# Kernel tuning notes

Measured on AMD Instinct MI355X. Metric: run time of the kernel, lower is better.

## Reference

```python
import jax, jax.numpy as jnp
import numpy as np

N_R, N_V, D, E_RR, L, G = 50000, 2000, 128, 800000, 3, 32


def setup_inputs() -> dict:
    key = jax.random.key(0)
    ks = jax.random.split(key, 10)
    x_real = jax.random.normal(ks[0], (N_R, D), dtype=jnp.float32)
    x_virtual = jax.random.normal(ks[1], (N_V, D), dtype=jnp.float32)
    # params: [num_layers, 3 relations (r_to_r, r_to_v, v_to_r), D, D]
    W_root = jax.random.normal(ks[2], (L, 3, D, D), dtype=jnp.float32) * 0.05
    W_nbr = jax.random.normal(ks[3], (L, 3, D, D), dtype=jnp.float32) * 0.05
    bias = jax.random.normal(ks[4], (L, 3, D), dtype=jnp.float32) * 0.05
    edge_rr = jax.random.randint(ks[5], (2, E_RR), 0, N_R)
    # one virtual-node edge per real node (hierarchical virtual nodes)
    src_rv = jnp.arange(N_R)
    dst_rv = jax.random.randint(ks[6], (N_R,), 0, N_V)
    edge_rv = jnp.stack([src_rv, dst_rv])          # real -> virtual
    edge_vr = jnp.stack([dst_rv, src_rv])          # virtual -> real
    batch_real = jnp.sort(jax.random.randint(ks[7], (N_R,), 0, G))
    return {
        "x_real": x_real, "x_virtual": x_virtual,
        "W_root": W_root, "W_nbr": W_nbr, "bias": bias,
        "edge_rr": edge_rr, "edge_rv": edge_rv, "edge_vr": edge_vr,
        "batch_real": batch_real,
    }


def _graph_conv(x_src, x_dst, src, dst, Wr, Wn, b, n_dst):
    # PyG GraphConv-style: root transform + sum-aggregated neighbor messages
    msg = jax.ops.segment_sum(x_src[src] @ Wn, dst, num_segments=n_dst)
    return x_dst @ Wr + msg + b


def _forward(x_real, x_virtual, W_root, W_nbr, bias, edge_rr, edge_rv, edge_vr, batch_real):
    x_r, x_v = x_real, x_virtual
    n_r, n_v = x_r.shape[0], x_v.shape[0]
    for l in range(W_root.shape[0]):
        # HeteroConv with aggr='sum': sum relation outputs per destination type
        c_rr = _graph_conv(x_r, x_r, edge_rr[0], edge_rr[1], W_root[l, 0], W_nbr[l, 0], bias[l, 0], n_r)
        c_vr = _graph_conv(x_v, x_r, edge_vr[0], edge_vr[1], W_root[l, 2], W_nbr[l, 2], bias[l, 2], n_r)
        c_rv = _graph_conv(x_r, x_v, edge_rv[0], edge_rv[1], W_root[l, 1], W_nbr[l, 1], bias[l, 1], n_v)
        # activation + dropout (eval mode -> identity)
        x_r = jax.nn.relu(c_rr + c_vr)
        x_v = jax.nn.relu(c_rv)
    # mean readout over real nodes per graph
    counts = jax.ops.segment_sum(jnp.ones((n_r,), x_r.dtype), batch_real, num_segments=G)
    graph_emb = jax.ops.segment_sum(x_r, batch_real, num_segments=G) / jnp.maximum(counts, 1.0)[:, None]
    return x_r, graph_emb


def reference(x_real, x_virtual, W_root, W_nbr, bias, edge_rr, edge_rv, edge_vr, batch_real):
    node_embedding, graph_embedding = _forward(
        x_real, x_virtual, W_root, W_nbr, bias, edge_rr, edge_rv, edge_vr, batch_real)
    return node_embedding, graph_embedding
```

## Files before the change

### kernel.cpp

```cpp
#include <hip/hip_runtime.h>
#include <hip/hip_bf16.h>

#define N_R   50000
#define N_V   2000
#define DIM   128
#define E_RR  800000
#define EPAD  (E_RR + 4 * N_R)
#define NLAY  3
#define NGR   32
#define RCHUNK 16

#define BUKD  128
#define NBUK  391
#define CHKE  2048
#define NCHK  391

typedef __attribute__((ext_vector_type(8))) short bf16x8;
typedef __attribute__((ext_vector_type(4))) float f32x4;
typedef __attribute__((ext_vector_type(2))) float f32x2;
typedef __attribute__((ext_vector_type(8))) unsigned char u8x8;

__device__ __forceinline__ ushort f2bf(float f) {
    unsigned u = __builtin_bit_cast(unsigned, f);
    unsigned r = (u + 0x7fffu + ((u >> 16) & 1u)) >> 16;
    return (ushort)r;
}
__device__ __forceinline__ float bf2f(ushort h) {
    unsigned u = ((unsigned)h) << 16;
    return __builtin_bit_cast(float, u);
}
__device__ __forceinline__ int lbound(const int* __restrict__ a, int n, int key) {
    int lo = 0, hi = n;
    while (lo < hi) { int mid = (lo + hi) >> 1; if (a[mid] < key) lo = mid + 1; else hi = mid; }
    return lo;
}

__device__ __forceinline__ void acc_u8row(
    unsigned w0, unsigned w1, float s,
    f32x2& a01, f32x2& a23, f32x2& a45, f32x2& a67)
{
    f32x2 sc = {s, s};
    a01 += sc * (f32x2){(float)(w0 & 0xffu), (float)((w0 >> 8) & 0xffu)};
    a23 += sc * (f32x2){(float)((w0 >> 16) & 0xffu), (float)(w0 >> 24)};
    a45 += sc * (f32x2){(float)(w1 & 0xffu), (float)((w1 >> 8) & 0xffu)};
    a67 += sc * (f32x2){(float)((w1 >> 16) & 0xffu), (float)(w1 >> 24)};
}

__global__ __launch_bounds__(256) void hist_kernel(
    const int* __restrict__ dst, int n, int* __restrict__ cnt)
{
    int i = blockIdx.x * 256 + threadIdx.x;
    if (i < n) atomicAdd(&cnt[dst[i]], 1);
}

__global__ __launch_bounds__(256) void scan_single_kernel(
    const int* __restrict__ cnt, int n, int nedges,
    int* __restrict__ rowptr, int* __restrict__ cursor)
{
    __shared__ int lds[256];
    __shared__ int carry;
    int t = threadIdx.x;
    if (t == 0) carry = 0;
    __syncthreads();
    for (int base = 0; base < n; base += 256) {
        int i = base + t;
        int v = (i < n) ? cnt[i] : 0;
        lds[t] = v;
        __syncthreads();
        #pragma unroll
        for (int off = 1; off < 256; off <<= 1) {
            int u = (t >= off) ? lds[t - off] : 0;
            __syncthreads();
            lds[t] += u;
            __syncthreads();
        }
        int excl = carry + lds[t] - v;
        if (i < n) {
            rowptr[i] = excl;
            if (cursor) cursor[i] = excl;
        }
        __syncthreads();
        if (t == 255) carry += lds[255];
        __syncthreads();
    }
    if (t == 0) rowptr[n] = (nedges >= 0) ? nedges : carry;
}

__global__ __launch_bounds__(256) void fill_kernel(
    const int* __restrict__ src, const int* __restrict__ dst, int n,
    int* __restrict__ cursor, int* __restrict__ col)
{
    int i = blockIdx.x * 256 + threadIdx.x;
    if (i < n) {
        int p = atomicAdd(&cursor[dst[i]], 1);
        col[p] = src[i];
    }
}

__global__ __launch_bounds__(256) void bkt_count_kernel(
    const int* __restrict__ dst, unsigned short* __restrict__ cnt2d)
{
    __shared__ int h[NBUK];
    int t = threadIdx.x, c = blockIdx.x;
    for (int i = t; i < NBUK; i += 256) h[i] = 0;
    __syncthreads();
    int e0 = c * CHKE, e1 = min(e0 + CHKE, E_RR);
    for (int e = e0 + t; e < e1; e += 256) atomicAdd(&h[dst[e] >> 7], 1);
    __syncthreads();
    for (int i = t; i < NBUK; i += 256)
        cnt2d[(size_t)c * NBUK + i] = (unsigned short)h[i];
}

__global__ __launch_bounds__(64) void bkt_prefix_kernel(
    const unsigned short* __restrict__ cnt2d,
    unsigned short* __restrict__ rel2d, int* __restrict__ tot)
{
    int b = blockIdx.x, lane = threadIdx.x;
    int base = 0;
    for (int c0 = 0; c0 < NCHK; c0 += 64) {
        int c = c0 + lane;
        int v = (c < NCHK) ? (int)cnt2d[(size_t)c * NBUK + b] : 0;
        int s = v;
        #pragma unroll
        for (int off = 1; off < 64; off <<= 1) {
            int u = __shfl_up(s, off);
            if (lane >= off) s += u;
        }
        if (c < NCHK) rel2d[(size_t)c * NBUK + b] = (unsigned short)(base + s - v);
        base += __shfl(s, 63);
    }
    if (lane == 0) tot[b] = base;
}

__global__ __launch_bounds__(256) void bkt_scatter_kernel(
    const int* __restrict__ src, const int* __restrict__ dst,
    const unsigned short* __restrict__ rel2d, const int* __restrict__ bstart,
    unsigned* __restrict__ ebuf)
{
    __shared__ int cur[NBUK];
    int t = threadIdx.x, c = blockIdx.x;
    for (int i = t; i < NBUK; i += 256)
        cur[i] = bstart[i] + (int)rel2d[(size_t)c * NBUK + i];
    __syncthreads();
    int e0 = c * CHKE, e1 = min(e0 + CHKE, E_RR);
    for (int e = e0 + t; e < e1; e += 256) {
        int d = dst[e];
        int p = atomicAdd(&cur[d >> 7], 1);
        ebuf[p] = ((unsigned)d << 16) | (unsigned)src[e];
    }
}

__global__ __launch_bounds__(256) void bkt_fineA_kernel(
    const unsigned* __restrict__ ebuf, const int* __restrict__ bstart,
    unsigned short* __restrict__ rowcnt, int* __restrict__ ptot)
{
    __shared__ int cnt[BUKD];
    __shared__ int red[BUKD];
    int b = blockIdx.x, t = threadIdx.x;
    int s0 = bstart[b], s1 = bstart[b + 1];
    if (t < BUKD) cnt[t] = 0;
    __syncthreads();
    for (int e = s0 + t; e < s1; e += 256)
        atomicAdd(&cnt[(ebuf[e] >> 16) & (BUKD - 1)], 1);
    __syncthreads();
    if (t < BUKD) {
        rowcnt[(size_t)b * BUKD + t] = (unsigned short)cnt[t];
        red[t] = (cnt[t] + 3) & ~3;
    }
    __syncthreads();
    #pragma unroll
    for (int off = 64; off > 0; off >>= 1) {
        if (t < off) red[t] += red[t + off];
        __syncthreads();
    }
    if (t == 0) ptot[b] = red[0];
}

__global__ __launch_bounds__(256) void bkt_fineB_kernel(
    const unsigned* __restrict__ ebuf, const int* __restrict__ bstart,
    const int* __restrict__ pbstart, const unsigned short* __restrict__ rowcnt,
    int* __restrict__ rowptr, unsigned short* __restrict__ col16)
{
    __shared__ int sc[BUKD];
    __shared__ int cur[BUKD];
    __shared__ int fend[BUKD];
    __shared__ int pend[BUKD];
    int b = blockIdx.x, t = threadIdx.x;
    int s0 = bstart[b], s1 = bstart[b + 1];
    int p0 = pbstart[b];
    int c = (t < BUKD) ? (int)rowcnt[(size_t)b * BUKD + t] : 0;
    int pc = (c + 3) & ~3;
    if (t < BUKD) sc[t] = pc;
    __syncthreads();
    #pragma unroll
    for (int off = 1; off < BUKD; off <<= 1) {
        int v = (t < BUKD && t >= off) ? sc[t - off] : 0;
        __syncthreads();
        if (t < BUKD) sc[t] += v;
        __syncthreads();
    }
    if (t < BUKD) {
        int ex = sc[t] - pc;
        int d = b * BUKD + t;
        if (d < N_R) rowptr[d] = p0 + ex;
        cur[t] = ex;
        fend[t] = ex + c;
        pend[t] = ex + pc;
    }
    if (b == NBUK - 1 && t == 0) rowptr[N_R] = pbstart[NBUK];
    __syncthreads();
    for (int e = s0 + t; e < s1; e += 256) {
        unsigned pk = ebuf[e];
        int p = atomicAdd(&cur[(pk >> 16) & (BUKD - 1)], 1);
        col16[p0 + p] = (unsigned short)(pk & 0xffffu);
    }
    __syncthreads();
    if (t < BUKD) {
        for (int p = fend[t]; p < pend[t]; ++p)
            col16[p0 + p] = 0xFFFFu;
    }
}

__global__ __launch_bounds__(256) void quant_input_kernel(
    const float* __restrict__ in, unsigned char* __restrict__ q,
    unsigned short* __restrict__ sbf)
{
    int w = (blockIdx.x * 256 + threadIdx.x) >> 6;
    int lane = threadIdx.x & 63;
    if (w >= N_R) return;
    float2 v = *(const float2*)(in + (size_t)w * DIM + lane * 2);
    float mx = fmaxf(fabsf(v.x), fabsf(v.y));
    #pragma unroll
    for (int off = 1; off < 64; off <<= 1)
        mx = fmaxf(mx, __shfl_xor(mx, off));
    ushort sb = f2bf(mx / 127.f);
    float s = bf2f(sb);
    float inv = (s > 0.f) ? 1.f / s : 0.f;
    int q0 = min(255, max(0, __float2int_rn(v.x * inv) + 128));
    int q1 = min(255, max(0, __float2int_rn(v.y * inv) + 128));
    *(ushort*)(q + (size_t)w * DIM + lane * 2) = (ushort)(q0 | (q1 << 8));
    if (lane == 0) sbf[w] = sb;
}

__global__ __launch_bounds__(256) void build_wt_kernel(
    const float* __restrict__ Wroot, const float* __restrict__ Wnbr,
    ushort* __restrict__ WT)
{
    int idx = blockIdx.x * 256 + threadIdx.x;
    if (idx >= NLAY * DIM * 2 * DIM) return;
    int k = idx & 255;
    int n = (idx >> 8) & 127;
    int l = idx >> 15;
    float v;
    if (k < DIM) {
        const float* base = Wroot + (size_t)l * 3 * DIM * DIM;
        v = base[(size_t)k * DIM + n] + base[(size_t)(2 * DIM + k) * DIM + n];
    } else {
        v = Wnbr[((size_t)l * 3 * DIM + (k - DIM)) * DIM + n];
    }
    WT[idx] = f2bf(v);
}

__global__ __launch_bounds__(256) void combine_b_kernel(
    const float* __restrict__ bias, float* __restrict__ bc)
{
    int idx = blockIdx.x * 256 + threadIdx.x;
    if (idx >= NLAY * DIM) return;
    int l = idx / DIM;
    int rest = idx - l * DIM;
    const float* base = bias + (size_t)l * 3 * DIM;
    bc[idx] = base[rest] + base[2 * DIM + rest];
}

__global__ __launch_bounds__(256) void vlayer_kernel(
    const int* __restrict__ rowptr_rr, const unsigned short* __restrict__ col16,
    unsigned* __restrict__ colp,
    const int* __restrict__ rowptr, const int* __restrict__ col,
    const unsigned char* __restrict__ Xq, const unsigned short* __restrict__ sbf,
    float zp, const float* __restrict__ xv,
    const float* __restrict__ Wn2, const float* __restrict__ Wr1,
    const float* __restrict__ Wn1, const float* __restrict__ b1,
    float* __restrict__ Tv, float* __restrict__ xv_next, int doNext)
{
    __shared__ float part[4 * DIM];
    __shared__ float arv_s[DIM];
    int v = blockIdx.x;
    int t = threadIdx.x;
    int wave = t >> 6, lane = t & 63;

    {
        int ptot = rowptr_rr[N_R];
        for (int i = v * 256 + t; i < ptot; i += N_V * 256) {
            unsigned c = col16[i];
            colp[i] = (c == 0xFFFFu) ? 0u : (c | ((unsigned)sbf[c] << 16));
        }
    }

    if (doNext) {
        int beg = rowptr[v], end = rowptr[v + 1];
        float a0 = 0.f, a1 = 0.f, ssum = 0.f;
        for (int e = beg + wave; e < end; e += 4) {
            int c = col[e];
            float s = bf2f(sbf[c]);
            uchar2 u = *(const uchar2*)(Xq + (size_t)c * DIM + lane * 2);
            a0 += s * (float)u.x;
            a1 += s * (float)u.y;
            ssum += s;
        }
        part[wave * DIM + lane * 2 + 0] = a0 - zp * ssum;
        part[wave * DIM + lane * 2 + 1] = a1 - zp * ssum;
        __syncthreads();
        if (t < DIM)
            arv_s[t] = part[t] + part[DIM + t] + part[2 * DIM + t] + part[3 * DIM + t];
        __syncthreads();
    }

    const float* arow = xv + (size_t)v * DIM;
    if (t < DIM) {
        float tacc = 0.f;
        #pragma unroll 8
        for (int k = 0; k < DIM; ++k)
            tacc += arow[k] * Wn2[(size_t)k * DIM + t];
        Tv[(size_t)v * DIM + t] = tacc;
    } else if (doNext) {
        int c = t - DIM;
        float nacc = 0.f;
        #pragma unroll 4
        for (int k = 0; k < DIM; ++k)
            nacc += arow[k] * Wr1[(size_t)k * DIM + c]
                  + arv_s[k] * Wn1[(size_t)k * DIM + c];
        xv_next[(size_t)v * DIM + c] = fmaxf(nacc + b1[c], 0.f);
    }
}

__global__ __launch_bounds__(256) void fused_layer_kernel(
    const int* __restrict__ rowptr, const unsigned* __restrict__ colp,
    const unsigned char* __restrict__ Xq, const unsigned short* __restrict__ sbf,
    float zp, const ushort* __restrict__ WT,
    const float* __restrict__ Tv,  const int* __restrict__ vmap,
    const float* __restrict__ bias,
    float* __restrict__ outF,
    unsigned char* __restrict__ Xq_out, unsigned short* __restrict__ sbf_out, int M)
{
    __shared__ ushort a2[16 * DIM];
    __shared__ float ost[16 * DIM];
    int t = threadIdx.x;

    int wave = t >> 6, lane = t & 63;
    int rlo = lane & 15, hi = lane >> 4;
    int row0 = blockIdx.x * 16;
    int arowc = min(row0 + rlo, M - 1);
    float sa = bf2f(sbf[arowc]);
    bf16x8 afr[8];
    #pragma unroll
    for (int j = 0; j < 4; ++j) {
        u8x8 uv = *(const u8x8*)(Xq + (size_t)arowc * DIM + 32 * j + 8 * hi);
        bf16x8 f;
        #pragma unroll
        for (int q = 0; q < 8; ++q)
            f[q] = (short)f2bf(sa * ((float)uv[q] - zp));
        afr[j] = f;
    }
    int vr[4];
    #pragma unroll
    for (int i = 0; i < 4; ++i)
        vr[i] = vmap[min(row0 + 4 * hi + i, M - 1)];

    {
        int g = t >> 3;
        int li = t & 7;
        int row = g >> 1;
        int half = g & 1;
        int drow = min(row0 + row, M - 1);
        int beg = rowptr[drow], end = rowptr[drow + 1];
        const unsigned char* XH = Xq + half * 64 + li * 8;
        f32x2 a01 = {0.f, 0.f}, a23 = {0.f, 0.f};
        f32x2 a45 = {0.f, 0.f}, a67 = {0.f, 0.f};
        float ssum = 0.f;
        for (int e = beg; e < end; e += 4) {
            uint4 p = *(const uint4*)(colp + e);
            float s0 = bf2f((ushort)(p.x >> 16)), s1 = bf2f((ushort)(p.y >> 16));
            float s2 = bf2f((ushort)(p.z >> 16)), s3 = bf2f((ushort)(p.w >> 16));
            uint2 d0 = *(const uint2*)(XH + (size_t)(p.x & 0xffffu) * DIM);
            uint2 d1 = *(const uint2*)(XH + (size_t)(p.y & 0xffffu) * DIM);
            uint2 d2 = *(const uint2*)(XH + (size_t)(p.z & 0xffffu) * DIM);
            uint2 d3 = *(const uint2*)(XH + (size_t)(p.w & 0xffffu) * DIM);
            acc_u8row(d0.x, d0.y, s0, a01, a23, a45, a67);
            acc_u8row(d1.x, d1.y, s1, a01, a23, a45, a67);
            acc_u8row(d2.x, d2.y, s2, a01, a23, a45, a67);
            acc_u8row(d3.x, d3.y, s3, a01, a23, a45, a67);
            ssum += (s0 + s1) + (s2 + s3);
        }
        float zs = zp * ssum;
        bf16x8 pk;
        pk[0] = (short)f2bf(a01.x - zs);
        pk[1] = (short)f2bf(a01.y - zs);
        pk[2] = (short)f2bf(a23.x - zs);
        pk[3] = (short)f2bf(a23.y - zs);
        pk[4] = (short)f2bf(a45.x - zs);
        pk[5] = (short)f2bf(a45.y - zs);
        pk[6] = (short)f2bf(a67.x - zs);
        pk[7] = (short)f2bf(a67.y - zs);
        int byte = row * 256 + ((half * 128 + li * 16) ^ ((row & 7) << 4));
        *(bf16x8*)((char*)a2 + byte) = pk;
    }
    __syncthreads();

    #pragma unroll
    for (int jj = 0; jj < 4; ++jj) {
        int byte = rlo * 256 + ((64 * jj + 16 * hi) ^ ((rlo & 7) << 4));
        afr[4 + jj] = *(const bf16x8*)((const char*)a2 + byte);
    }

    f32x4 acc[2];
    #pragma unroll
    for (int n = 0; n < 2; ++n) acc[n] = (f32x4){0.f, 0.f, 0.f, 0.f};

    #pragma unroll
    for (int n = 0; n < 2; ++n) {
        int nt = wave * 2 + n;
        const ushort* wrow = WT + (size_t)(nt * 16 + rlo) * (2 * DIM);
        #pragma unroll
        for (int j = 0; j < 8; ++j) {
            bf16x8 bfr = *(const bf16x8*)(wrow + 32 * j + 8 * hi);
            acc[n] = __builtin_amdgcn_mfma_f32_16x16x32_bf16(afr[j], bfr, acc[n], 0, 0, 0);
        }
    }

    if (outF) {
        #pragma unroll
        for (int n = 0; n < 2; ++n) {
            int ncol = (wave * 2 + n) * 16 + rlo;
            float bv = bias[ncol];
            #pragma unroll
            for (int i = 0; i < 4; ++i) {
                int orow = row0 + 4 * hi + i;
                if (orow >= M) continue;
                float v = acc[n][i] + bv + Tv[(size_t)vr[i] * DIM + ncol];
                outF[(size_t)orow * DIM + ncol] = fmaxf(v, 0.f);
            }
        }
    } else {
        #pragma unroll
        for (int n = 0; n < 2; ++n) {
            int ncol = (wave * 2 + n) * 16 + rlo;
            float bv = bias[ncol];
            #pragma unroll
            for (int i = 0; i < 4; ++i) {
                float v = acc[n][i] + bv + Tv[(size_t)vr[i] * DIM + ncol];
                ost[(4 * hi + i) * DIM + ncol] = fmaxf(v, 0.f);
            }
        }
        __syncthreads();
        int g16 = t >> 4;
        int li16 = t & 15;
        int orow = row0 + g16;
        float4 f0 = *(const float4*)(ost + g16 * DIM + li16 * 8);
        float4 f1 = *(const float4*)(ost + g16 * DIM + li16 * 8 + 4);
        float mx = fmaxf(fmaxf(fmaxf(f0.x, f0.y), fmaxf(f0.z, f0.w)),
                         fmaxf(fmaxf(f1.x, f1.y), fmaxf(f1.z, f1.w)));
        #pragma unroll
        for (int off = 1; off < 16; off <<= 1)
            mx = fmaxf(mx, __shfl_xor(mx, off, 16));
        ushort sb = f2bf(mx / 255.f);
        float s = bf2f(sb);
        float inv = (s > 0.f) ? 1.f / s : 0.f;
        if (orow < M) {
            u8x8 qv;
            qv[0] = (unsigned char)min(255, __float2int_rn(f0.x * inv));
            qv[1] = (unsigned char)min(255, __float2int_rn(f0.y * inv));
            qv[2] = (unsigned char)min(255, __float2int_rn(f0.z * inv));
            qv[3] = (unsigned char)min(255, __float2int_rn(f0.w * inv));
            qv[4] = (unsigned char)min(255, __float2int_rn(f1.x * inv));
            qv[5] = (unsigned char)min(255, __float2int_rn(f1.y * inv));
            qv[6] = (unsigned char)min(255, __float2int_rn(f1.z * inv));
            qv[7] = (unsigned char)min(255, __float2int_rn(f1.w * inv));
            *(u8x8*)(Xq_out + (size_t)orow * DIM + li16 * 8) = qv;
            if (li16 == 0) sbf_out[orow] = sb;
        }
    }
}

__global__ __launch_bounds__(256) void readout_kernel(
    const float* __restrict__ xr, const int* __restrict__ batch,
    float* __restrict__ gsum, int nrows)
{
    __shared__ float lds[256 * 4];
    int g = blockIdx.x / RCHUNK;
    int chunk = blockIdx.x % RCHUNK;
    int lo = lbound(batch, nrows, g);
    int hi = lbound(batch, nrows, g + 1);
    int len = hi - lo;
    if (len == 0) return;
    int per = (len + RCHUNK - 1) / RCHUNK;
    int r0 = lo + chunk * per;
    int r1 = min(r0 + per, hi);

    int t = threadIdx.x;
    int c4 = (t & 31) << 2;
    int rsub = t >> 5;

    float4 acc = make_float4(0.f, 0.f, 0.f, 0.f);
    for (int r = r0 + rsub; r < r1; r += 8) {
        float4 v = *(const float4*)(xr + (size_t)r * DIM + c4);
        acc.x += v.x; acc.y += v.y; acc.z += v.z; acc.w += v.w;
    }
    *(float4*)(lds + t * 4) = acc;
    __syncthreads();
    if (rsub == 0) {
        float4 s = make_float4(0.f, 0.f, 0.f, 0.f);
        #pragma unroll
        for (int j = 0; j < 8; ++j) {
            float4 v = *(const float4*)(lds + (j * 32 + t) * 4);
            s.x += v.x; s.y += v.y; s.z += v.z; s.w += v.w;
        }
        atomicAdd(&gsum[(size_t)g * DIM + c4 + 0], s.x);
        atomicAdd(&gsum[(size_t)g * DIM + c4 + 1], s.y);
        atomicAdd(&gsum[(size_t)g * DIM + c4 + 2], s.z);
        atomicAdd(&gsum[(size_t)g * DIM + c4 + 3], s.w);
    }
}

__global__ __launch_bounds__(256) void finalize_kernel(
    const float* __restrict__ gsum, const int* __restrict__ batch,
    float* __restrict__ out, int nrows)
{
    int idx = blockIdx.x * 256 + threadIdx.x;
    if (idx >= NGR * DIM) return;
    int g = idx >> 7;
    int lo = lbound(batch, nrows, g);
    int hi = lbound(batch, nrows, g + 1);
    float c = fmaxf((float)(hi - lo), 1.f);
    out[idx] = gsum[idx] / c;
}

extern "C" void kernel_launch(void* const* d_in, const int* in_sizes, int n_in,
                              void* d_out, int out_size, void* d_ws, size_t ws_size,
                              hipStream_t stream)
{
    const float* x_real    = (const float*)d_in[0];
    const float* x_virtual = (const float*)d_in[1];
    const float* W_root    = (const float*)d_in[2];
    const float* W_nbr     = (const float*)d_in[3];
    const float* bias      = (const float*)d_in[4];
    const int*   edge_rr   = (const int*)d_in[5];
    const int*   edge_rv   = (const int*)d_in[6];
    const int*   edge_vr   = (const int*)d_in[7];
    const int*   batch     = (const int*)d_in[8];

    float* out = (float*)d_out;

    float*  ws    = (float*)d_ws;
    float*  Tv    = ws;
    float*  xv_a  = Tv   + (size_t)N_V * DIM;
    float*  xv_b  = xv_a + (size_t)N_V * DIM;
    float*  bc    = xv_b + (size_t)N_V * DIM;
    float*  gsum  = bc   + (size_t)NLAY * DIM;
    ushort* WT    = (ushort*)(gsum + NGR * DIM);
    unsigned* colp = (unsigned*)(WT + (size_t)NLAY * DIM * 2 * DIM);
    unsigned* ebuf = colp + EPAD;
    int* iws       = (int*)(ebuf + E_RR);
    int* rowptr_rr = iws;
    int* cnt_v     = rowptr_rr + N_R + 1;
    int* rowptr_rv = cnt_v + N_V;
    int* cursor_rv = rowptr_rv + N_V + 1;
    int* col_rv    = cursor_rv + N_V;
    int* tot       = col_rv + N_R;
    int* bstart    = tot + NBUK;
    int* ptot      = bstart + NBUK + 1;
    int* pbstart   = ptot + NBUK;
    unsigned short* col16 = (unsigned short*)(pbstart + NBUK + 1);
    unsigned short* cnt2d = col16 + EPAD;
    unsigned short* rel2d = cnt2d + (size_t)NCHK * NBUK;
    unsigned short* rowcnt = rel2d + (size_t)NCHK * NBUK;
    unsigned short* sbf0  = rowcnt + (size_t)NBUK * BUKD;
    unsigned short* sbf1  = sbf0 + N_R;
    unsigned short* sbf2  = sbf1 + N_R;
    unsigned char* Q0 = (unsigned char*)(sbf2 + N_R);
    unsigned char* Q1 = Q0 + (size_t)N_R * DIM;
    unsigned char* Q2 = Q1 + (size_t)N_R * DIM;

    const int* rr_src = edge_rr;
    const int* rr_dst = edge_rr + E_RR;
    const int* rv_src = edge_rv;
    const int* rv_dst = edge_rv + N_R;

    bkt_count_kernel<<<NCHK, 256, 0, stream>>>(rr_dst, cnt2d);
    bkt_prefix_kernel<<<NBUK, 64, 0, stream>>>(cnt2d, rel2d, tot);
    scan_single_kernel<<<1, 256, 0, stream>>>(tot, NBUK, E_RR, bstart, nullptr);
    bkt_scatter_kernel<<<NCHK, 256, 0, stream>>>(rr_src, rr_dst, rel2d, bstart, ebuf);
    bkt_fineA_kernel<<<NBUK, 256, 0, stream>>>(ebuf, bstart, rowcnt, ptot);
    scan_single_kernel<<<1, 256, 0, stream>>>(ptot, NBUK, -1, pbstart, nullptr);
    bkt_fineB_kernel<<<NBUK, 256, 0, stream>>>(ebuf, bstart, pbstart, rowcnt,
                                               rowptr_rr, col16);

    hipMemsetAsync(cnt_v, 0, (size_t)N_V * sizeof(int), stream);
    hist_kernel<<<(N_R + 255) / 256, 256, 0, stream>>>(rv_dst, N_R, cnt_v);
    scan_single_kernel<<<1, 256, 0, stream>>>(cnt_v, N_V, N_R, rowptr_rv, cursor_rv);
    fill_kernel<<<(N_R + 255) / 256, 256, 0, stream>>>(rv_src, rv_dst, N_R, cursor_rv, col_rv);

    build_wt_kernel<<<(NLAY * DIM * 2 * DIM + 255) / 256, 256, 0, stream>>>(W_root, W_nbr, WT);
    combine_b_kernel<<<(NLAY * DIM + 255) / 256, 256, 0, stream>>>(bias, bc);
    quant_input_kernel<<<(N_R * 64 + 255) / 256, 256, 0, stream>>>(x_real, Q0, sbf0);

    unsigned char* Qcur = Q0;  unsigned short* Scur = sbf0;
    const float* cur_xv = x_virtual;

    for (int l = 0; l < NLAY; ++l) {
        const float* Wn1 = W_nbr + ((size_t)l * 3 + 1) * DIM * DIM;
        const float* Wn2 = W_nbr + ((size_t)l * 3 + 2) * DIM * DIM;
        const float* Wr1 = W_root + ((size_t)l * 3 + 1) * DIM * DIM;
        const float* b1  = bias + ((size_t)l * 3 + 1) * DIM;

        int doNext = (l < NLAY - 1);
        float zp = (l == 0) ? 128.f : 0.f;
        float* xv_out = (l & 1) ? xv_b : xv_a;

        vlayer_kernel<<<N_V, 256, 0, stream>>>(
            rowptr_rr, col16, colp,
            rowptr_rv, col_rv, Qcur, Scur, zp, cur_xv,
            Wn2, Wr1, Wn1, b1, Tv, xv_out, doNext);

        unsigned char*  Qnext = (l == 0) ? Q1 : Q2;
        unsigned short* Snext = (l == 0) ? sbf1 : sbf2;
        float* outF = (l == NLAY - 1) ? out : nullptr;
        fused_layer_kernel<<<(N_R + 15) / 16, 256, 0, stream>>>(
            rowptr_rr, colp, Qcur, Scur, zp, WT + (size_t)l * DIM * 2 * DIM,
            Tv, edge_vr, bc + (size_t)l * DIM,
            outF, outF ? nullptr : Qnext, outF ? nullptr : Snext, N_R);

        if (doNext) { cur_xv = xv_out; Qcur = Qnext; Scur = Snext; }
    }

    hipMemsetAsync(gsum, 0, (size_t)NGR * DIM * sizeof(float), stream);
    readout_kernel<<<NGR * RCHUNK, 256, 0, stream>>>(out, batch, gsum, N_R);
    finalize_kernel<<<(NGR * DIM + 255) / 256, 256, 0, stream>>>(
        gsum, batch, out + (size_t)N_R * DIM, N_R);
}
```

Measured before the change: 317.4 us.

## Sort destination rows by degree to balance fused layer work

Builds a permutation of real nodes bucketed by in-degree, using a histogram, a scan and an atomic scatter, and makes the fused layer kernel process rows in that order. The aim is that the 16 rows in each block have similar edge counts, so the gather loop wastes less time waiting on its longest row. It adds small preprocessing kernels and indirect row indexing. Row reads and writes become scattered instead of contiguous, which may hurt memory coalescing.

```diff
diff --git a/kernel.cpp b/kernel.cpp
--- a/kernel.cpp
+++ b/kernel.cpp
@@ -218,6 +218,28 @@
     if (t < BUKD) {
         for (int p = fend[t]; p < pend[t]; ++p)
             col16[p0 + p] = 0xFFFFu;
+    }
+}
+
+__global__ __launch_bounds__(256) void deg_hist_kernel(
+    const int* __restrict__ rowptr, int* __restrict__ dh)
+{
+    int i = blockIdx.x * 256 + threadIdx.x;
+    if (i < N_R) {
+        int d = min(255, (rowptr[i + 1] - rowptr[i]) >> 2);
+        atomicAdd(&dh[d], 1);
+    }
+}
+
+__global__ __launch_bounds__(256) void deg_scatter_kernel(
+    const int* __restrict__ rowptr, int* __restrict__ cursor,
+    int* __restrict__ perm)
+{
+    int i = blockIdx.x * 256 + threadIdx.x;
+    if (i < N_R) {
+        int d = min(255, (rowptr[i + 1] - rowptr[i]) >> 2);
+        int p = atomicAdd(&cursor[d], 1);
+        perm[p] = i;
     }
 }
 
@@ -335,6 +357,7 @@
 
 __global__ __launch_bounds__(256) void fused_layer_kernel(
     const int* __restrict__ rowptr, const unsigned* __restrict__ colp,
+    const int* __restrict__ perm,
     const unsigned char* __restrict__ Xq, const unsigned short* __restrict__ sbf,
     float zp, const ushort* __restrict__ WT,
     const float* __restrict__ Tv,  const int* __restrict__ vmap,
@@ -349,7 +372,7 @@
     int wave = t >> 6, lane = t & 63;
     int rlo = lane & 15, hi = lane >> 4;
     int row0 = blockIdx.x * 16;
-    int arowc = min(row0 + rlo, M - 1);
+    int arowc = perm[min(row0 + rlo, M - 1)];
     float sa = bf2f(sbf[arowc]);
     bf16x8 afr[8];
     #pragma unroll
@@ -361,17 +384,20 @@
             f[q] = (short)f2bf(sa * ((float)uv[q] - zp));
         afr[j] = f;
     }
+    int pr[4];
     int vr[4];
     #pragma unroll
-    for (int i = 0; i < 4; ++i)
-        vr[i] = vmap[min(row0 + 4 * hi + i, M - 1)];
+    for (int i = 0; i < 4; ++i) {
+        pr[i] = perm[min(row0 + 4 * hi + i, M - 1)];
+        vr[i] = vmap[pr[i]];
+    }
 
     {
         int g = t >> 3;
         int li = t & 7;
         int row = g >> 1;
         int half = g & 1;
-        int drow = min(row0 + row, M - 1);
+        int drow = perm[min(row0 + row, M - 1)];
         int beg = rowptr[drow], end = rowptr[drow + 1];
         const unsigned char* XH = Xq + half * 64 + li * 8;
         f32x2 a01 = {0.f, 0.f}, a23 = {0.f, 0.f};
@@ -434,10 +460,9 @@
             float bv = bias[ncol];
             #pragma unroll
             for (int i = 0; i < 4; ++i) {
-                int orow = row0 + 4 * hi + i;
-                if (orow >= M) continue;
+                if (row0 + 4 * hi + i >= M) continue;
                 float v = acc[n][i] + bv + Tv[(size_t)vr[i] * DIM + ncol];
-                outF[(size_t)orow * DIM + ncol] = fmaxf(v, 0.f);
+                outF[(size_t)pr[i] * DIM + ncol] = fmaxf(v, 0.f);
             }
         }
     } else {
@@ -454,7 +479,6 @@
         __syncthreads();
         int g16 = t >> 4;
         int li16 = t & 15;
-        int orow = row0 + g16;
         float4 f0 = *(const float4*)(ost + g16 * DIM + li16 * 8);
         float4 f1 = *(const float4*)(ost + g16 * DIM + li16 * 8 + 4);
         float mx = fmaxf(fmaxf(fmaxf(f0.x, f0.y), fmaxf(f0.z, f0.w)),
@@ -465,7 +489,8 @@
         ushort sb = f2bf(mx / 255.f);
         float s = bf2f(sb);
         float inv = (s > 0.f) ? 1.f / s : 0.f;
-        if (orow < M) {
+        if (row0 + g16 < M) {
+            int orow = perm[row0 + g16];
             u8x8 qv;
             qv[0] = (unsigned char)min(255, __float2int_rn(f0.x * inv));
             qv[1] = (unsigned char)min(255, __float2int_rn(f0.y * inv));
@@ -569,7 +594,10 @@
     int* bstart    = tot + NBUK;
     int* ptot      = bstart + NBUK + 1;
     int* pbstart   = ptot + NBUK;
-    unsigned short* col16 = (unsigned short*)(pbstart + NBUK + 1);
+    int* perm      = pbstart + NBUK + 1;
+    int* dh        = perm + N_R;
+    int* dcur      = dh + 257;
+    unsigned short* col16 = (unsigned short*)(dcur + 256);
     unsigned short* cnt2d = col16 + EPAD;
     unsigned short* rel2d = cnt2d + (size_t)NCHK * NBUK;
     unsigned short* rowcnt = rel2d + (size_t)NCHK * NBUK;
@@ -594,6 +622,11 @@
     bkt_fineB_kernel<<<NBUK, 256, 0, stream>>>(ebuf, bstart, pbstart, rowcnt,
                                                rowptr_rr, col16);
 
+    hipMemsetAsync(dh, 0, 257 * sizeof(int), stream);
+    deg_hist_kernel<<<(N_R + 255) / 256, 256, 0, stream>>>(rowptr_rr, dh);
+    scan_single_kernel<<<1, 256, 0, stream>>>(dh, 256, -1, dh, dcur);
+    deg_scatter_kernel<<<(N_R + 255) / 256, 256, 0, stream>>>(rowptr_rr, dcur, perm);
+
     hipMemsetAsync(cnt_v, 0, (size_t)N_V * sizeof(int), stream);
     hist_kernel<<<(N_R + 255) / 256, 256, 0, stream>>>(rv_dst, N_R, cnt_v);
     scan_single_kernel<<<1, 256, 0, stream>>>(cnt_v, N_V, N_R, rowptr_rv, cursor_rv);
@@ -625,7 +658,7 @@
         unsigned short* Snext = (l == 0) ? sbf1 : sbf2;
         float* outF = (l == NLAY - 1) ? out : nullptr;
         fused_layer_kernel<<<(N_R + 15) / 16, 256, 0, stream>>>(
-            rowptr_rr, colp, Qcur, Scur, zp, WT + (size_t)l * DIM * 2 * DIM,
+            rowptr_rr, colp, perm, Qcur, Scur, zp, WT + (size_t)l * DIM * 2 * DIM,
             Tv, edge_vr, bc + (size_t)l * DIM,
             outF, outF ? nullptr : Qnext, outF ? nullptr : Snext, N_R);
 
```

Result: slower. 892.2 us (+181.1%).
